# Performance work log

Hardware: AMD Instinct MI355X
Metric: run time of the kernel (lower is better)

The kernel has to match this reference:

```python
import jax, jax.numpy as jnp
import numpy as np

B, S, D, H = 4, 2048, 1024, 16
DH = D // H  # head dim = dim_k = dim_v


def setup_inputs() -> dict:
    key = jax.random.key(0)
    ks = jax.random.split(key, 8)
    return {
        "query": jax.random.normal(ks[0], (B, S, D), jnp.float32),
        "key": jax.random.normal(ks[1], (B, S, D), jnp.float32),
        "value": jax.random.normal(ks[2], (B, S, D), jnp.float32),
        # per-head projection weights, stacked over heads: [H, D, DH]
        "Wq": jax.random.normal(ks[3], (H, D, DH), jnp.float32) / np.sqrt(D),
        "Wk": jax.random.normal(ks[4], (H, D, DH), jnp.float32) / np.sqrt(D),
        "Wv": jax.random.normal(ks[5], (H, D, DH), jnp.float32) / np.sqrt(D),
        "Wo": jax.random.normal(ks[6], (D, D), jnp.float32) / np.sqrt(D),
        "bo": jax.random.normal(ks[7], (D,), jnp.float32) * 0.01,
        "is_causal": 1,
    }


def reference(query, key, value, Wq, Wk, Wv, Wo, bo, is_causal):
    # Per-head projections, batched over heads via einsum.  [B,H,S,DH]
    q = jnp.einsum("bsd,hdk->bhsk", query, Wq)
    k = jnp.einsum("bsd,hdk->bhsk", key, Wk)
    v = jnp.einsum("bsd,hdk->bhsk", value, Wv)
    scores = jnp.einsum("bhqk,bhsk->bhqs", q, k) / jnp.sqrt(jnp.float32(DH))
    if is_causal:
        mask = jnp.triu(jnp.ones((S, S), bool), k=1)  # strict upper tri
        scores = jnp.where(mask, -jnp.inf, scores)
    attn = jax.nn.softmax(scores, axis=-1)
    out = jnp.einsum("bhqs,bhsk->bhqk", attn, v)
    # concat heads along last dim == [B,S,H*DH], then output projection
    out = out.transpose(0, 2, 1, 3).reshape(B, S, D)
    return out @ Wo.T + bo
```

## Files before the change

kernel.cpp:

```cpp
#include <hip/hip_runtime.h>
#include <hip/hip_bf16.h>
#include <stdint.h>

typedef __bf16 bf16_t;
typedef __bf16 bf16x8 __attribute__((ext_vector_type(8)));
typedef float  f32x4  __attribute__((ext_vector_type(4)));

#define B_   4
#define S_   2048
#define D_   1024
#define H_   16
#define DH_  64
#define MTOT (B_ * S_)
#define NITEMS 1024
#define NPERS  768

__device__ __forceinline__ void gload_lds16(const void* g, void* l) {
  __builtin_amdgcn_global_load_lds((const __attribute__((address_space(1))) void*)g,
                                   (__attribute__((address_space(3))) void*)l,
                                   16, 0, 0);
}

__global__ __launch_bounds__(256) void k_cvt(const float* __restrict__ in,
                                             bf16_t* __restrict__ out, int n8) {
  for (int i = blockIdx.x * blockDim.x + threadIdx.x; i < n8;
       i += gridDim.x * blockDim.x) {
    const float4* p = (const float4*)(in + (size_t)i * 8);
    float4 a = p[0], b = p[1];
    bf16x8 o;
    o[0] = (bf16_t)a.x; o[1] = (bf16_t)a.y; o[2] = (bf16_t)a.z; o[3] = (bf16_t)a.w;
    o[4] = (bf16_t)b.x; o[5] = (bf16_t)b.y; o[6] = (bf16_t)b.z; o[7] = (bf16_t)b.w;
    *(bf16x8*)(out + (size_t)i * 8) = o;
  }
}

__global__ __launch_bounds__(256) void k_pack(const float* __restrict__ Wq,
                                              const float* __restrict__ Wk,
                                              const float* __restrict__ Wv,
                                              bf16_t* __restrict__ Wt) {
  const int z = blockIdx.z;
  const float* W = (z == 0) ? Wq : ((z == 1) ? Wk : Wv);
  const float scale = (z == 0) ? 0.125f : 1.0f;
  const int h  = blockIdx.y;
  const int d0 = blockIdx.x * 64;

  __shared__ float tile[64][65];
  const int t  = threadIdx.x;
  const int r  = t >> 2;
  const int c0 = (t & 3) * 16;

  const float* src = W + ((size_t)h * D_ + d0 + r) * DH_ + c0;
#pragma unroll
  for (int j4 = 0; j4 < 4; ++j4) {
    float4 v = *(const float4*)(src + j4 * 4);
    tile[r][c0 + j4 * 4 + 0] = v.x;
    tile[r][c0 + j4 * 4 + 1] = v.y;
    tile[r][c0 + j4 * 4 + 2] = v.z;
    tile[r][c0 + j4 * 4 + 3] = v.w;
  }
  __syncthreads();

  const int kk = r, dd0 = c0;
  bf16_t* dst = Wt + ((size_t)z * D_ + h * DH_ + kk) * D_ + d0 + dd0;
  bf16x8 o0, o1;
#pragma unroll
  for (int j = 0; j < 8; ++j) {
    o0[j] = (bf16_t)(tile[dd0 + j][kk] * scale);
    o1[j] = (bf16_t)(tile[dd0 + 8 + j][kk] * scale);
  }
  *(bf16x8*)(dst)     = o0;
  *(bf16x8*)(dst + 8) = o1;
}

template <int MODE>
__global__ __launch_bounds__(256) void k_gemm(
    const bf16_t* __restrict__ A0, const bf16_t* __restrict__ A1,
    const bf16_t* __restrict__ A2, const bf16_t* __restrict__ W,
    bf16_t* __restrict__ O0, bf16_t* __restrict__ O1, bf16_t* __restrict__ O2,
    float* __restrict__ OF, const float* __restrict__ bias,
    int M, int N, int K) {
  const int z = blockIdx.z;
  const bf16_t* A  = (MODE == 0) ? (z == 0 ? A0 : (z == 1 ? A1 : A2)) : A0;
  const bf16_t* Bt = (MODE == 0) ? (W + (size_t)z * N * K) : W;
  bf16_t* OB = (MODE == 0) ? (z == 0 ? O0 : (z == 1 ? O1 : O2)) : nullptr;

  __shared__ bf16_t As[128 * 32];
  __shared__ bf16_t Bs[128 * 32];

  const int tid  = threadIdx.x;
  const int w    = tid >> 6, lane = tid & 63;
  const int wm   = w >> 1,   wn   = w & 1;
  const int g    = lane >> 4, cl  = lane & 15;
  const int m0   = blockIdx.x * 128, n0 = blockIdx.y * 128;
  const int r_a  = lane >> 2;
  const int c_a  = (lane & 3) * 8;

  f32x4 acc[4][4] = {};

  for (int k0 = 0; k0 < K; k0 += 32) {
#pragma unroll
    for (int it = 0; it < 2; ++it) {
      const int c16 = it * 4 + w;
      const int row = c16 * 16 + r_a;
      gload_lds16(A  + (size_t)(m0 + row) * K + (k0 + c_a),
                  (bf16_t*)((char*)As + c16 * 1024));
      gload_lds16(Bt + (size_t)(n0 + row) * K + (k0 + c_a),
                  (bf16_t*)((char*)Bs + c16 * 1024));
    }
    __syncthreads();

    bf16x8 af[4], bfv[4];
#pragma unroll
    for (int mi = 0; mi < 4; ++mi)
      af[mi] = *(const bf16x8*)&As[(wm * 64 + mi * 16 + cl) * 32 + g * 8];
#pragma unroll
    for (int ni = 0; ni < 4; ++ni)
      bfv[ni] = *(const bf16x8*)&Bs[(wn * 64 + ni * 16 + cl) * 32 + g * 8];
#pragma unroll
    for (int mi = 0; mi < 4; ++mi)
#pragma unroll
      for (int ni = 0; ni < 4; ++ni)
        acc[mi][ni] = __builtin_amdgcn_mfma_f32_16x16x32_bf16(
            af[mi], bfv[ni], acc[mi][ni], 0, 0, 0);
    __syncthreads();
  }

#pragma unroll
  for (int mi = 0; mi < 4; ++mi) {
#pragma unroll
    for (int ni = 0; ni < 4; ++ni) {
      const int col = n0 + wn * 64 + ni * 16 + cl;
#pragma unroll
      for (int i = 0; i < 4; ++i) {
        const int row = m0 + wm * 64 + mi * 16 + g * 4 + i;
        if (MODE == 0)
          OB[(size_t)row * N + col] = (bf16_t)acc[mi][ni][i];
        else
          OF[(size_t)row * N + col] = acc[mi][ni][i] + bias[col];
      }
    }
  }
}

__global__ __launch_bounds__(256, 3) void k_attn(const bf16_t* __restrict__ Qp,
                                                 const bf16_t* __restrict__ Kp,
                                                 const bf16_t* __restrict__ Vp,
                                                 bf16_t* __restrict__ AO,
                                                 int* __restrict__ wq_ctr,
                                                 const int* __restrict__ causal_p) {
  __shared__ bf16_t Ks[64 * 72];
  __shared__ bf16_t Vs[2 * 64 * 64];
  __shared__ bf16_t Vt[64 * 72];
  __shared__ bf16_t Pb[4][32 * 72];
  __shared__ int s_item;

  const int tid  = threadIdx.x;
  const int w    = tid >> 6, lane = tid & 63;
  const int g    = lane >> 4, cl  = lane & 15;
  const int causal = *causal_p;

  bf16x8 ones;
#pragma unroll
  for (int j = 0; j < 8; ++j) ones[j] = (bf16_t)1.0f;

  const int kr  = tid >> 3;
  const int kc  = (tid & 7) * 8;
  const int vd  = tid & 63;
  const int vk0 = w * 16;

  for (;;) {
    if (tid == 0) s_item = atomicAdd(wq_ctr, 1);
    __syncthreads();
    const int item = s_item;
    if (item >= NITEMS) break;

    const int qb = 15 - (item >> 6);
    const int bh = item & 63;
    const int b  = bh >> 4, h = bh & 15;
    const int q0 = qb * 128;
    const int nt = causal ? (2 * qb + 2) : (S_ >> 6);
    const int base_q = q0 + w * 32;
    const size_t base = ((size_t)b * S_) * D_ + (size_t)h * DH_;

    bf16x8 aq[2][2];
#pragma unroll
    for (int qi = 0; qi < 2; ++qi)
#pragma unroll
      for (int ks = 0; ks < 2; ++ks)
        aq[qi][ks] = *(const bf16x8*)(Qp + base + (size_t)(base_q + qi * 16 + cl) * D_ +
                                      ks * 32 + g * 8);

    f32x4 acc_o[2][4] = {};
    float m_run[2][4], l_run[2][4];
#pragma unroll
    for (int qi = 0; qi < 2; ++qi)
#pragma unroll
      for (int i = 0; i < 4; ++i) { m_run[qi][i] = -1e30f; l_run[qi][i] = 0.f; }

    bf16x8 kreg[2];
    kreg[0] = *(const bf16x8*)(Kp + base + (size_t)(kr) * D_ + kc);
    kreg[1] = *(const bf16x8*)(Kp + base + (size_t)(32 + kr) * D_ + kc);
#pragma unroll
    for (int it = 0; it < 2; ++it) {
      const int c16 = it * 4 + w;
      gload_lds16(Vp + base + (size_t)(c16 * 8 + (lane >> 3)) * D_ + (lane & 7) * 8,
                  (char*)Vs + c16 * 1024);
    }
    *(bf16x8*)&Ks[(kr) * 72 + kc]      = kreg[0];
    *(bf16x8*)&Ks[(32 + kr) * 72 + kc] = kreg[1];
    __syncthreads();

    for (int t = 0; t < nt; ++t) {
      const int kv0 = t * 64;
      const int buf = t & 1;
      const bool pf = (t + 1 < nt);

      if (pf) {
        const int kvn = kv0 + 64;
        kreg[0] = *(const bf16x8*)(Kp + base + (size_t)(kvn + kr) * D_ + kc);
        kreg[1] = *(const bf16x8*)(Kp + base + (size_t)(kvn + 32 + kr) * D_ + kc);
#pragma unroll
        for (int it = 0; it < 2; ++it) {
          const int c16 = it * 4 + w;
          gload_lds16(Vp + base + (size_t)(kvn + c16 * 8 + (lane >> 3)) * D_ + (lane & 7) * 8,
                      (char*)Vs + (buf ^ 1) * 8192 + c16 * 1024);
        }
      }

      {
        const bf16_t* vsb = Vs + buf * 4096;
        bf16x8 w0, w1;
#pragma unroll
        for (int j = 0; j < 8; ++j) {
          w0[j] = vsb[(vk0 + j) * 64 + vd];
          w1[j] = vsb[(vk0 + 8 + j) * 64 + vd];
        }
        *(bf16x8*)&Vt[vd * 72 + vk0]     = w0;
        *(bf16x8*)&Vt[vd * 72 + vk0 + 8] = w1;
      }

      const bool active    = (!causal) || (kv0 <= base_q + 31);
      const bool need_mask = causal && (kv0 + 63 > base_q);

      if (active) {
        f32x4 sc[2][4];
#pragma unroll
        for (int qi = 0; qi < 2; ++qi)
#pragma unroll
          for (int c = 0; c < 4; ++c) sc[qi][c] = (f32x4){0.f, 0.f, 0.f, 0.f};

        __builtin_amdgcn_s_setprio(1);
#pragma unroll
        for (int c = 0; c < 4; ++c) {
          bf16x8 kf0 = *(const bf16x8*)&Ks[(c * 16 + cl) * 72 + g * 8];
          bf16x8 kf1 = *(const bf16x8*)&Ks[(c * 16 + cl) * 72 + 32 + g * 8];
#pragma unroll
          for (int qi = 0; qi < 2; ++qi) {
            sc[qi][c] = __builtin_amdgcn_mfma_f32_16x16x32_bf16(aq[qi][0], kf0, sc[qi][c], 0, 0, 0);
            sc[qi][c] = __builtin_amdgcn_mfma_f32_16x16x32_bf16(aq[qi][1], kf1, sc[qi][c], 0, 0, 0);
          }
        }
        __builtin_amdgcn_s_setprio(0);

        if (need_mask) {
#pragma unroll
          for (int qi = 0; qi < 2; ++qi)
#pragma unroll
            for (int c = 0; c < 4; ++c)
#pragma unroll
              for (int i = 0; i < 4; ++i) {
                const int qg = base_q + qi * 16 + g * 4 + i;
                const int kg = kv0 + c * 16 + cl;
                if (kg > qg) sc[qi][c][i] = -1e30f;
              }
        }

#pragma unroll
        for (int qi = 0; qi < 2; ++qi) {
          float alpha[4];
#pragma unroll
          for (int i = 0; i < 4; ++i) {
            float m1 = fmaxf(fmaxf(sc[qi][0][i], sc[qi][1][i]),
                             fmaxf(sc[qi][2][i], sc[qi][3][i]));
            m1 = fmaxf(m1, __shfl_xor(m1, 1));
            m1 = fmaxf(m1, __shfl_xor(m1, 2));
            m1 = fmaxf(m1, __shfl_xor(m1, 4));
            m1 = fmaxf(m1, __shfl_xor(m1, 8));
            const float mnew = fmaxf(m_run[qi][i], m1);
            alpha[i] = exp2f((m_run[qi][i] - mnew) * 1.44269504f);
            m_run[qi][i] = mnew;
          }
#pragma unroll
          for (int i = 0; i < 4; ++i) {
            l_run[qi][i] *= alpha[i];
            acc_o[qi][0][i] *= alpha[i];
            acc_o[qi][1][i] *= alpha[i];
            acc_o[qi][2][i] *= alpha[i];
            acc_o[qi][3][i] *= alpha[i];
          }
#pragma unroll
          for (int c = 0; c < 4; ++c)
#pragma unroll
            for (int i = 0; i < 4; ++i) {
              const float p = exp2f((sc[qi][c][i] - m_run[qi][i]) * 1.44269504f);
              Pb[w][(qi * 16 + g * 4 + i) * 72 + c * 16 + cl] = (bf16_t)p;
            }
        }
      }

      __syncthreads();

      if (pf) {
        *(bf16x8*)&Ks[(kr) * 72 + kc]      = kreg[0];
        *(bf16x8*)&Ks[(32 + kr) * 72 + kc] = kreg[1];
      }

      if (active) {
        f32x4 sacc[2] = {};
        __builtin_amdgcn_s_setprio(1);
#pragma unroll
        for (int ks = 0; ks < 2; ++ks) {
          bf16x8 pa0 = *(const bf16x8*)&Pb[w][(cl) * 72 + ks * 32 + g * 8];
          bf16x8 pa1 = *(const bf16x8*)&Pb[w][(16 + cl) * 72 + ks * 32 + g * 8];
          sacc[0] = __builtin_amdgcn_mfma_f32_16x16x32_bf16(pa0, ones, sacc[0], 0, 0, 0);
          sacc[1] = __builtin_amdgcn_mfma_f32_16x16x32_bf16(pa1, ones, sacc[1], 0, 0, 0);
#pragma unroll
          for (int dg = 0; dg < 4; ++dg) {
            bf16x8 vf = *(const bf16x8*)&Vt[(dg * 16 + cl) * 72 + ks * 32 + g * 8];
            acc_o[0][dg] = __builtin_amdgcn_mfma_f32_16x16x32_bf16(pa0, vf, acc_o[0][dg], 0, 0, 0);
            acc_o[1][dg] = __builtin_amdgcn_mfma_f32_16x16x32_bf16(pa1, vf, acc_o[1][dg], 0, 0, 0);
          }
        }
        __builtin_amdgcn_s_setprio(0);
#pragma unroll
        for (int qi = 0; qi < 2; ++qi)
#pragma unroll
          for (int i = 0; i < 4; ++i) l_run[qi][i] += sacc[qi][i];
      }

      __syncthreads();
    }

#pragma unroll
    for (int qi = 0; qi < 2; ++qi)
#pragma unroll
      for (int dg = 0; dg < 4; ++dg)
#pragma unroll
        for (int i = 0; i < 4; ++i) {
          const int q = base_q + qi * 16 + g * 4 + i;
          AO[base + (size_t)q * D_ + dg * 16 + cl] = (bf16_t)(acc_o[qi][dg][i] / l_run[qi][i]);
        }
  }
}

extern "C" void kernel_launch(void* const* d_in, const int* in_sizes, int n_in,
                              void* d_out, int out_size, void* d_ws, size_t ws_size,
                              hipStream_t stream) {
  const float* query = (const float*)d_in[0];
  const float* key_  = (const float*)d_in[1];
  const float* value = (const float*)d_in[2];
  const float* Wq    = (const float*)d_in[3];
  const float* Wk    = (const float*)d_in[4];
  const float* Wv    = (const float*)d_in[5];
  const float* Wo    = (const float*)d_in[6];
  const float* bo    = (const float*)d_in[7];
  const int*   causal = (const int*)d_in[8];
  float* out = (float*)d_out;

  char* ws = (char*)d_ws;
  size_t off = 0;
  auto alloc = [&](size_t bytes) {
    char* p = ws + off;
    off += (bytes + 255) & ~(size_t)255;
    return p;
  };
  const size_t TB = (size_t)MTOT * D_ * sizeof(bf16_t);
  bf16_t* qin = (bf16_t*)alloc(TB);
  bf16_t* kin = (bf16_t*)alloc(TB);
  bf16_t* vin = (bf16_t*)alloc(TB);
  bf16_t* Qp  = (bf16_t*)alloc(TB);
  bf16_t* Kp  = (bf16_t*)alloc(TB);
  bf16_t* Vp  = (bf16_t*)alloc(TB);
  bf16_t* wt  = (bf16_t*)alloc((size_t)3 * D_ * D_ * sizeof(bf16_t));
  bf16_t* wob = (bf16_t*)alloc((size_t)D_ * D_ * sizeof(bf16_t));
  int*    ctr = (int*)alloc(256);
  bf16_t* ao  = qin;

  hipMemsetAsync(ctr, 0, sizeof(int), stream);

  const int n8 = MTOT * D_ / 8;
  k_cvt<<<2048, 256, 0, stream>>>(query, qin, n8);
  k_cvt<<<2048, 256, 0, stream>>>(key_,  kin, n8);
  k_cvt<<<2048, 256, 0, stream>>>(value, vin, n8);
  k_cvt<<<512, 256, 0, stream>>>(Wo, wob, D_ * D_ / 8);
  k_pack<<<dim3(16, 16, 3), 256, 0, stream>>>(Wq, Wk, Wv, wt);

  k_gemm<0><<<dim3(MTOT / 128, D_ / 128, 3), 256, 0, stream>>>(
      qin, kin, vin, wt, Qp, Kp, Vp, nullptr, nullptr, MTOT, D_, D_);

  k_attn<<<dim3(NPERS, 1), 256, 0, stream>>>(Qp, Kp, Vp, ao, ctr, causal);

  k_gemm<1><<<dim3(MTOT / 128, D_ / 128, 1), 256, 0, stream>>>(
      ao, nullptr, nullptr, wob, nullptr, nullptr, nullptr, out, bo, MTOT, D_, D_);
}
```

Measured before the change: 389.2 us.

## Transpose QK^T MFMA layout, add lazy max rescaling, compute row sums in registers

Swaps the MFMA operand order so each lane holds one query row's scores across keys. The row max then needs only two cross-lane shuffles, and P can be written to LDS as packed bf16x4 stores. Rescaling of the output accumulator is skipped unless some row's max grows by more than a threshold, in the style of FA4. Row sums are accumulated from the fp32 probabilities in registers instead of through an extra MFMA against a ones vector. The lazy rescale and the fp32-versus-bf16 sum change the numerics slightly, and there are added shuffles to broadcast alpha and l to the output layout.

```diff
diff --git a/kernel.cpp b/kernel.cpp
--- a/kernel.cpp
+++ b/kernel.cpp
@@ -3,6 +3,7 @@
 #include <stdint.h>
 
 typedef __bf16 bf16_t;
+typedef __bf16 bf16x4 __attribute__((ext_vector_type(4)));
 typedef __bf16 bf16x8 __attribute__((ext_vector_type(8)));
 typedef float  f32x4  __attribute__((ext_vector_type(4)));
 
@@ -158,10 +159,7 @@
   const int w    = tid >> 6, lane = tid & 63;
   const int g    = lane >> 4, cl  = lane & 15;
   const int causal = *causal_p;
-
-  bf16x8 ones;
-#pragma unroll
-  for (int j = 0; j < 8; ++j) ones[j] = (bf16_t)1.0f;
+  const int gbase = (lane & 48) | ((lane & 48) >> 2);
 
   const int kr  = tid >> 3;
   const int kc  = (tid & 7) * 8;
@@ -191,11 +189,9 @@
                                       ks * 32 + g * 8);
 
     f32x4 acc_o[2][4] = {};
-    float m_run[2][4], l_run[2][4];
-#pragma unroll
-    for (int qi = 0; qi < 2; ++qi)
-#pragma unroll
-      for (int i = 0; i < 4; ++i) { m_run[qi][i] = -1e30f; l_run[qi][i] = 0.f; }
+    float m_run[2], l_run[2];
+#pragma unroll
+    for (int qi = 0; qi < 2; ++qi) { m_run[qi] = -1e30f; l_run[qi] = 0.f; }
 
     bf16x8 kreg[2];
     kreg[0] = *(const bf16x8*)(Kp + base + (size_t)(kr) * D_ + kc);
@@ -256,55 +252,65 @@
           bf16x8 kf1 = *(const bf16x8*)&Ks[(c * 16 + cl) * 72 + 32 + g * 8];
 #pragma unroll
           for (int qi = 0; qi < 2; ++qi) {
-            sc[qi][c] = __builtin_amdgcn_mfma_f32_16x16x32_bf16(aq[qi][0], kf0, sc[qi][c], 0, 0, 0);
-            sc[qi][c] = __builtin_amdgcn_mfma_f32_16x16x32_bf16(aq[qi][1], kf1, sc[qi][c], 0, 0, 0);
+            sc[qi][c] = __builtin_amdgcn_mfma_f32_16x16x32_bf16(kf0, aq[qi][0], sc[qi][c], 0, 0, 0);
+            sc[qi][c] = __builtin_amdgcn_mfma_f32_16x16x32_bf16(kf1, aq[qi][1], sc[qi][c], 0, 0, 0);
           }
         }
         __builtin_amdgcn_s_setprio(0);
 
         if (need_mask) {
 #pragma unroll
-          for (int qi = 0; qi < 2; ++qi)
+          for (int qi = 0; qi < 2; ++qi) {
+            const int qg = base_q + qi * 16 + cl;
 #pragma unroll
             for (int c = 0; c < 4; ++c)
 #pragma unroll
               for (int i = 0; i < 4; ++i) {
-                const int qg = base_q + qi * 16 + g * 4 + i;
-                const int kg = kv0 + c * 16 + cl;
+                const int kg = kv0 + c * 16 + g * 4 + i;
                 if (kg > qg) sc[qi][c][i] = -1e30f;
               }
+          }
         }
 
 #pragma unroll
         for (int qi = 0; qi < 2; ++qi) {
-          float alpha[4];
-#pragma unroll
-          for (int i = 0; i < 4; ++i) {
-            float m1 = fmaxf(fmaxf(sc[qi][0][i], sc[qi][1][i]),
-                             fmaxf(sc[qi][2][i], sc[qi][3][i]));
-            m1 = fmaxf(m1, __shfl_xor(m1, 1));
-            m1 = fmaxf(m1, __shfl_xor(m1, 2));
-            m1 = fmaxf(m1, __shfl_xor(m1, 4));
-            m1 = fmaxf(m1, __shfl_xor(m1, 8));
-            const float mnew = fmaxf(m_run[qi][i], m1);
-            alpha[i] = exp2f((m_run[qi][i] - mnew) * 1.44269504f);
-            m_run[qi][i] = mnew;
+          float m4[4];
+#pragma unroll
+          for (int c = 0; c < 4; ++c)
+            m4[c] = fmaxf(fmaxf(sc[qi][c][0], sc[qi][c][1]),
+                          fmaxf(sc[qi][c][2], sc[qi][c][3]));
+          float m1 = fmaxf(fmaxf(m4[0], m4[1]), fmaxf(m4[2], m4[3]));
+          m1 = fmaxf(m1, __shfl_xor(m1, 16));
+          m1 = fmaxf(m1, __shfl_xor(m1, 32));
+          if (!__all(m1 <= m_run[qi] + 8.0f)) {
+            const float mnew = fmaxf(m_run[qi], m1);
+            const float alpha = exp2f((m_run[qi] - mnew) * 1.44269504f);
+            m_run[qi] = mnew;
+            l_run[qi] *= alpha;
+#pragma unroll
+            for (int i = 0; i < 4; ++i) {
+              const float ai = __shfl(alpha, gbase + i);
+              acc_o[qi][0][i] *= ai;
+              acc_o[qi][1][i] *= ai;
+              acc_o[qi][2][i] *= ai;
+              acc_o[qi][3][i] *= ai;
+            }
           }
-#pragma unroll
-          for (int i = 0; i < 4; ++i) {
-            l_run[qi][i] *= alpha[i];
-            acc_o[qi][0][i] *= alpha[i];
-            acc_o[qi][1][i] *= alpha[i];
-            acc_o[qi][2][i] *= alpha[i];
-            acc_o[qi][3][i] *= alpha[i];
+          float s = 0.f;
+#pragma unroll
+          for (int c = 0; c < 4; ++c) {
+            bf16x4 pv;
+#pragma unroll
+            for (int i = 0; i < 4; ++i) {
+              const float p = exp2f((sc[qi][c][i] - m_run[qi]) * 1.44269504f);
+              s += p;
+              pv[i] = (bf16_t)p;
+            }
+            *(bf16x4*)&Pb[w][(qi * 16 + cl) * 72 + c * 16 + ((lane >> 2) & 12)] = pv;
           }
-#pragma unroll
-          for (int c = 0; c < 4; ++c)
-#pragma unroll
-            for (int i = 0; i < 4; ++i) {
-              const float p = exp2f((sc[qi][c][i] - m_run[qi][i]) * 1.44269504f);
-              Pb[w][(qi * 16 + g * 4 + i) * 72 + c * 16 + cl] = (bf16_t)p;
-            }
+          s += __shfl_xor(s, 16);
+          s += __shfl_xor(s, 32);
+          l_run[qi] += s;
         }
       }
 
@@ -316,14 +322,11 @@
       }
 
       if (active) {
-        f32x4 sacc[2] = {};
         __builtin_amdgcn_s_setprio(1);
 #pragma unroll
         for (int ks = 0; ks < 2; ++ks) {
           bf16x8 pa0 = *(const bf16x8*)&Pb[w][(cl) * 72 + ks * 32 + g * 8];
           bf16x8 pa1 = *(const bf16x8*)&Pb[w][(16 + cl) * 72 + ks * 32 + g * 8];
-          sacc[0] = __builtin_amdgcn_mfma_f32_16x16x32_bf16(pa0, ones, sacc[0], 0, 0, 0);
-          sacc[1] = __builtin_amdgcn_mfma_f32_16x16x32_bf16(pa1, ones, sacc[1], 0, 0, 0);
 #pragma unroll
           for (int dg = 0; dg < 4; ++dg) {
             bf16x8 vf = *(const bf16x8*)&Vt[(dg * 16 + cl) * 72 + ks * 32 + g * 8];
@@ -332,24 +335,24 @@
           }
         }
         __builtin_amdgcn_s_setprio(0);
-#pragma unroll
-        for (int qi = 0; qi < 2; ++qi)
-#pragma unroll
-          for (int i = 0; i < 4; ++i) l_run[qi][i] += sacc[qi][i];
       }
 
       __syncthreads();
     }
 
 #pragma unroll
-    for (int qi = 0; qi < 2; ++qi)
+    for (int qi = 0; qi < 2; ++qi) {
+      float lq[4];
+#pragma unroll
+      for (int i = 0; i < 4; ++i) lq[i] = __shfl(l_run[qi], gbase + i);
 #pragma unroll
       for (int dg = 0; dg < 4; ++dg)
 #pragma unroll
         for (int i = 0; i < 4; ++i) {
           const int q = base_q + qi * 16 + g * 4 + i;
-          AO[base + (size_t)q * D_ + dg * 16 + cl] = (bf16_t)(acc_o[qi][dg][i] / l_run[qi][i]);
-        }
+          AO[base + (size_t)q * D_ + dg * 16 + cl] = (bf16_t)(acc_o[qi][dg][i] / lq[i]);
+        }
+    }
   }
 }
 
```

After: 360.6 us. 7.3% less time.
